# Optimization experiments

Hardware: AMD Instinct MI355X
Metric: run time of the kernel (lower is better)

Reference implementation:

```python
import jax, jax.numpy as jnp
import numpy as np

N_NODES = 100000
N_EDGES = 1600000
IN_DIM = 160
HID = 128
BN_EPS = 1e-5


def setup_inputs() -> dict:
    key = jax.random.key(0)
    ks = jax.random.split(key, 16)
    d = {}
    d['x'] = jax.random.normal(ks[0], (N_NODES, IN_DIM), dtype=jnp.float32)
    d['edge_index'] = jax.random.randint(ks[1], (2, N_EDGES), 0, N_NODES, dtype=jnp.int64)
    dims = [(IN_DIM, HID), (HID, HID), (HID, HID)]
    for i, (fi, fo) in enumerate(dims):
        s = 1.0 / np.sqrt(fi)
        d[f'wl{i}'] = jax.random.normal(ks[2 + 4 * i], (fi, fo), dtype=jnp.float32) * s
        d[f'wr{i}'] = jax.random.normal(ks[3 + 4 * i], (fi, fo), dtype=jnp.float32) * s
        d[f'bl{i}'] = jnp.zeros((fo,), dtype=jnp.float32)
        d[f'g{i}'] = jnp.ones((fo,), dtype=jnp.float32)
        d[f'be{i}'] = jnp.zeros((fo,), dtype=jnp.float32)
        d[f'rm{i}'] = jax.random.normal(ks[4 + 4 * i], (fo,), dtype=jnp.float32) * 0.1
        d[f'rv{i}'] = jnp.ones((fo,), dtype=jnp.float32)
    d['lin_w'] = jax.random.normal(ks[14], (HID, 1), dtype=jnp.float32) * (1.0 / np.sqrt(HID))
    d['lin_b'] = jnp.zeros((1,), dtype=jnp.float32)
    return d


def _sage_bn_relu(h, src, dst, wl, wr, bl, g, be, rm, rv):
    # mean neighbor aggregation: gather messages at src, scatter-mean to dst
    msg = h[src]                                            # [E, d]
    agg = jax.ops.segment_sum(msg, dst, num_segments=N_NODES)
    cnt = jax.ops.segment_sum(jnp.ones((msg.shape[0],), h.dtype), dst, num_segments=N_NODES)
    mean = agg / jnp.maximum(cnt, 1.0)[:, None]             # nodes w/o in-edges -> 0
    out = mean @ wl + bl + h @ wr                           # SAGEConv (root_weight=True)
    # BatchNorm1d (inference: running stats) + ReLU
    out = (out - rm) * (g * jax.lax.rsqrt(rv + BN_EPS)) + be
    return jax.nn.relu(out)


def reference(x, edge_index,
              wl0, wr0, bl0, g0, be0, rm0, rv0,
              wl1, wr1, bl1, g1, be1, rm1, rv1,
              wl2, wr2, bl2, g2, be2, rm2, rv2,
              lin_w, lin_b):
    src, dst = edge_index[0], edge_index[1]
    h = _sage_bn_relu(x, src, dst, wl0, wr0, bl0, g0, be0, rm0, rv0)
    h = _sage_bn_relu(h, src, dst, wl1, wr1, bl1, g1, be1, rm1, rv1)
    h = _sage_bn_relu(h, src, dst, wl2, wr2, bl2, g2, be2, rm2, rv2)
    return (h @ lin_w + lin_b)[:, 0]                        # [N]
```

## Files before the change

kernel.cpp:

```cpp
#include <hip/hip_runtime.h>

#define N_NODES 100000
#define N_EDGES 1600000
#define IN_DIM 160
#define HID 128
#define BN_EPS 1e-5f

#define M_PAD 100096
#define NBUCK 196
#define BSH 9
#define EPB 8192
#define NHB (NBUCK * NBUCK)
#define LPAD 132

typedef unsigned int uint;
typedef unsigned short ushort;
typedef __attribute__((ext_vector_type(8))) short bf16x8;
typedef __attribute__((ext_vector_type(4))) float f32x4;
typedef __attribute__((ext_vector_type(2))) float f32x2;

__device__ __forceinline__ ushort bf16rn(float f) {
    uint u = __float_as_uint(f);
    u += 0x7fffu + ((u >> 16) & 1u);
    return (ushort)(u >> 16);
}
__device__ __forceinline__ float bflo(uint u) { return __uint_as_float(u << 16); }
__device__ __forceinline__ float bfhi(uint u) { return __uint_as_float(u & 0xffff0000u); }


__device__ __forceinline__ void prep_body(int ob, int lane, const float* __restrict__ wl,
                                          const float* __restrict__ wr,
                                          ushort* __restrict__ Bf, int K) {
    int kb = ob >> 4;
    int tt = ob & 15;
    int n = tt * 16 + (lane & 15);
    int k0 = kb * 32 + (lane >> 4) * 8;
    ushort* dst = Bf + ((size_t)(kb * 16 + tt) * 64 + lane) * 8;
#pragma unroll
    for (int e = 0; e < 8; ++e) {
        int k = k0 + e;
        float v = (n < HID) ? wl[k * HID + n] : wr[k * HID + (n - HID)];
        dst[e] = bf16rn(v);
    }
}

#define PREP0_B 20
#define PREP1_B 16
#define INIT_GRID (NBUCK + PREP0_B + 2 * PREP1_B + 2)

__global__ __launch_bounds__(256) void init_kernel(
    const int* __restrict__ dst, int* __restrict__ ghist,
    const float* __restrict__ wl0, const float* __restrict__ wr0,
    const float* __restrict__ wl1, const float* __restrict__ wr1,
    const float* __restrict__ wl2, const float* __restrict__ wr2,
    ushort* __restrict__ Bf0, ushort* __restrict__ Bf1, ushort* __restrict__ Bf2,
    const float* __restrict__ bl0, const float* __restrict__ g0,
    const float* __restrict__ be0, const float* __restrict__ rm0,
    const float* __restrict__ rv0,
    const float* __restrict__ bl1, const float* __restrict__ g1,
    const float* __restrict__ be1, const float* __restrict__ rm1,
    const float* __restrict__ rv1,
    const float* __restrict__ bl2, const float* __restrict__ g2,
    const float* __restrict__ be2, const float* __restrict__ rm2,
    const float* __restrict__ rv2,
    float* __restrict__ bnscale, float* __restrict__ bnshift) {
    __shared__ int hist[NBUCK];
    int b = blockIdx.x, t = threadIdx.x;
    if (b < NBUCK) {
        for (int i = t; i < NBUCK; i += 256) hist[i] = 0;
        __syncthreads();
        int e0 = b * EPB;
        for (int i = 0; i < EPB; i += 256) {
            int e = e0 + i + t;
            if (e < N_EDGES) atomicAdd(&hist[dst[e] >> BSH], 1);
        }
        __syncthreads();
        for (int i = t; i < NBUCK; i += 256) ghist[i * NBUCK + b] = hist[i];
    } else if (b < NBUCK + PREP0_B) {
        prep_body((b - NBUCK) * 4 + (t >> 6), t & 63, wl0, wr0, Bf0, IN_DIM);
    } else if (b < NBUCK + PREP0_B + PREP1_B) {
        prep_body((b - NBUCK - PREP0_B) * 4 + (t >> 6), t & 63, wl1, wr1, Bf1, HID);
    } else if (b < NBUCK + PREP0_B + 2 * PREP1_B) {
        prep_body((b - NBUCK - PREP0_B - PREP1_B) * 4 + (t >> 6), t & 63, wl2, wr2, Bf2, HID);
    } else {
        int tt = (b - (NBUCK + PREP0_B + 2 * PREP1_B)) * 256 + t;
        if (tt < 3 * HID) {
            int L = tt >> 7, j = tt & 127;
            const float* bl = (L == 0) ? bl0 : (L == 1) ? bl1 : bl2;
            const float* gg = (L == 0) ? g0  : (L == 1) ? g1  : g2;
            const float* be = (L == 0) ? be0 : (L == 1) ? be1 : be2;
            const float* rm = (L == 0) ? rm0 : (L == 1) ? rm1 : rm2;
            const float* rv = (L == 0) ? rv0 : (L == 1) ? rv1 : rv2;
            float s = gg[j] * rsqrtf(rv[j] + BN_EPS);
            bnscale[tt] = s;
            bnshift[tt] = (bl[j] - rm[j]) * s + be[j];
        }
    }
}

#define SPT 38

__global__ __launch_bounds__(1024) void scan_all_kernel(int* __restrict__ ghist,
                                                        int* __restrict__ gbb) {
    __shared__ int ts[1024];
    int t = threadIdx.x;
    int base = t * SPT;
    int v[SPT];
    int s = 0;
#pragma unroll
    for (int i = 0; i < SPT; ++i) {
        int idx = base + i;
        int x = (idx < NHB) ? ghist[idx] : 0;
        v[i] = s;
        s += x;
    }
    ts[t] = s;
    __syncthreads();
    for (int off = 1; off < 1024; off <<= 1) {
        int a = (t >= off) ? ts[t - off] : 0;
        __syncthreads();
        ts[t] += a;
        __syncthreads();
    }
    int ex = (t > 0) ? ts[t - 1] : 0;
#pragma unroll
    for (int i = 0; i < SPT; ++i) {
        int idx = base + i;
        if (idx < NHB) {
            int e = ex + v[i];
            ghist[idx] = e;
            if (idx % NBUCK == 0) gbb[idx / NBUCK] = e;
        }
    }
    if (t == 0) gbb[NBUCK] = N_EDGES;
}


__global__ __launch_bounds__(256) void bucket_csr_kernel(const uint* __restrict__ scat,
                                                         const int* __restrict__ gbb,
                                                         int* __restrict__ prow,
                                                         int* __restrict__ deg,
                                                         int* __restrict__ peidx) {
    __shared__ int cnt[512], fl[512], pref[512];
    __shared__ int ts[256];
    __shared__ int tot_s;
    int b = blockIdx.x, t = threadIdx.x;
    int beg = gbb[b], end = gbb[b + 1];
    int pb = beg + b * 8192;
    cnt[t] = 0; cnt[t + 256] = 0;
    __syncthreads();
    for (int i = beg + t; i < end; i += 256)
        atomicAdd(&cnt[scat[i] >> 17], 1);
    __syncthreads();
    int c0 = cnt[2 * t], c1 = cnt[2 * t + 1];
    int p0 = (c0 + 15) & ~15, p1 = (c1 + 15) & ~15;
    ts[t] = p0 + p1;
    __syncthreads();
    for (int off = 1; off < 256; off <<= 1) {
        int v = (t >= off) ? ts[t - off] : 0;
        __syncthreads();
        ts[t] += v;
        __syncthreads();
    }
    int ex = (t > 0) ? ts[t - 1] : 0;
    pref[2 * t] = ex;
    pref[2 * t + 1] = ex + p0;
    fl[t] = 0; fl[t + 256] = 0;
    if (t == 255) tot_s = ts[255];
    int g0 = b * 512 + 2 * t;
    if (g0 < N_NODES) { prow[g0] = pb + ex; deg[g0] = c0; }
    if (g0 + 1 < N_NODES) { prow[g0 + 1] = pb + ex + p0; deg[g0 + 1] = c1; }
    __syncthreads();
    int tot = tot_s;
    for (int i = t; i < tot; i += 256) peidx[pb + i] = N_NODES;
    __syncthreads();
    for (int i = beg + t; i < end; i += 256) {
        uint w = scat[i];
        int nl = (int)(w >> 17);
        int lp = atomicAdd(&fl[nl], 1);
        peidx[pb + pref[nl] + lp] = (int)(w & 0x1FFFFu);
    }
}

template <int K, bool AFP32>
__device__ __forceinline__ void gemm_body(int bx, int t, ushort* ldsA,
                                          const void* __restrict__ A_,
                                          const ushort* __restrict__ Bf,
                                          ushort* __restrict__ tl,
                                          ushort* __restrict__ troot) {
    constexpr int CPR = K / 8;
    constexpr int FULLG = CPR & ~7;
    const int m0b = bx * 64;

#pragma unroll
    for (int i = 0; i < (64 * CPR) / 256; ++i) {
        int cidx = i * 256 + t;
        int row = cidx / CPR;
        int j = cidx - row * CPR;
        bf16x8 v;
        if (AFP32) {
            const float* A = (const float*)A_;
            int m = m0b + row;
            float4 f0 = make_float4(0.f, 0.f, 0.f, 0.f), f1 = f0;
            if (m < N_NODES) {
                f0 = *(const float4*)(A + (size_t)m * K + j * 8);
                f1 = *(const float4*)(A + (size_t)m * K + j * 8 + 4);
            }
            v[0] = (short)bf16rn(f0.x); v[1] = (short)bf16rn(f0.y);
            v[2] = (short)bf16rn(f0.z); v[3] = (short)bf16rn(f0.w);
            v[4] = (short)bf16rn(f1.x); v[5] = (short)bf16rn(f1.y);
            v[6] = (short)bf16rn(f1.z); v[7] = (short)bf16rn(f1.w);
        } else {
            const ushort* A = (const ushort*)A_;
            v = *(const bf16x8*)(A + (size_t)(m0b + row) * K + j * 8);
        }
        int swz = (j < FULLG) ? ((j & ~7) | ((j ^ row) & 7))
                              : ((j & ~3) | ((j ^ row) & 3));
        *(bf16x8*)&ldsA[row * K + swz * 8] = v;
    }
    __syncthreads();

    const int lane = t & 63;
    const int wv = t >> 6;
    const int col = lane & 15;
    const int q = lane >> 4;
    const int rh = wv & 1;
    const int ch = wv >> 1;
    const int row0 = rh * 32 + col;
    f32x4 acc0[8], acc1[8];
#pragma unroll
    for (int tt = 0; tt < 8; ++tt) {
        acc0[tt] = (f32x4){0.f, 0.f, 0.f, 0.f};
        acc1[tt] = (f32x4){0.f, 0.f, 0.f, 0.f};
    }

#pragma unroll
    for (int kb = 0; kb < K / 32; ++kb) {
        int jj = kb * 4 + q;
        int swzj = (jj < FULLG) ? ((jj & ~7) | ((jj ^ col) & 7))
                                : ((jj & ~3) | ((jj ^ col) & 3));
        bf16x8 a0 = *(const bf16x8*)&ldsA[row0 * K + swzj * 8];
        bf16x8 a1 = *(const bf16x8*)&ldsA[(row0 + 16) * K + swzj * 8];
        const ushort* bp = Bf + ((size_t)((kb * 16 + ch * 8) * 64) + lane) * 8;
#pragma unroll
        for (int tt = 0; tt < 8; ++tt) {
            bf16x8 bfr = *(const bf16x8*)(bp + (size_t)tt * 64 * 8);
            acc0[tt] = __builtin_amdgcn_mfma_f32_16x16x32_bf16(a0, bfr, acc0[tt], 0, 0, 0);
            acc1[tt] = __builtin_amdgcn_mfma_f32_16x16x32_bf16(a1, bfr, acc1[tt], 0, 0, 0);
        }
    }

    __syncthreads();
    ushort(*rp)[16][LPAD] = (ushort(*)[16][LPAD])ldsA;
    ushort* outp = ch ? troot : tl;
#pragma unroll
    for (int mt = 0; mt < 2; ++mt) {
        const f32x4* ac = mt ? acc1 : acc0;
#pragma unroll
        for (int tt = 0; tt < 8; ++tt)
#pragma unroll
            for (int r = 0; r < 4; ++r)
                rp[wv][q * 4 + r][tt * 16 + col] = bf16rn(ac[tt][r]);
        int mbase = m0b + rh * 32 + mt * 16;
#pragma unroll
        for (int i = 0; i < 4; ++i) {
            int lin = i * 64 + lane;
            int row = lin >> 4;
            int c16 = lin & 15;
            bf16x8 v = *(const bf16x8*)&rp[wv][row][c16 * 8];
            *(bf16x8*)(outp + (size_t)(mbase + row) * HID + c16 * 8) = v;
        }
    }
}

__global__ __launch_bounds__(256) void scatter_gemm1_kernel(
    const int* __restrict__ src, const int* __restrict__ dst,
    const int* __restrict__ ghist, uint* __restrict__ scat,
    const float* __restrict__ x, const ushort* __restrict__ Bf0,
    ushort* __restrict__ tl, ushort* __restrict__ troot) {
    constexpr int LDSE = (64 * IN_DIM > 4 * 16 * LPAD) ? 64 * IN_DIM : 4 * 16 * LPAD;
    __shared__ ushort ldsA[LDSE];
    int b = blockIdx.x, t = threadIdx.x;
    if (b < NBUCK) {
        int* base = (int*)ldsA;
        int* fill = base + NBUCK;
        for (int i = t; i < NBUCK; i += 256) { base[i] = ghist[i * NBUCK + b]; fill[i] = 0; }
        __syncthreads();
        int e0 = b * EPB;
        for (int i = 0; i < EPB; i += 256) {
            int e = e0 + i + t;
            if (e < N_EDGES) {
                int d = dst[e];
                int sv = src[e];
                int bk = d >> BSH;
                int lp = atomicAdd(&fill[bk], 1);
                scat[base[bk] + lp] = (uint)sv | ((uint)(d & 511) << 17);
            }
        }
    } else {
        gemm_body<IN_DIM, true>(b - NBUCK, t, ldsA, x, Bf0, tl, troot);
    }
}

__global__ __launch_bounds__(256) void fused_agg_gemm_kernel(
    const ushort* __restrict__ tl_in, const ushort* __restrict__ troot_in,
    const int* __restrict__ prow, const int* __restrict__ deg_,
    const int* __restrict__ peidx,
    const float* __restrict__ bnscale, const float* __restrict__ bnshift,
    const ushort* __restrict__ Bf,
    ushort* __restrict__ tl_out, ushort* __restrict__ troot_out) {
    constexpr int K = HID;
    constexpr int LDSE = (64 * K > 4 * 16 * LPAD) ? 64 * K : 4 * 16 * LPAD;
    __shared__ ushort ldsA[LDSE];
    const int t = threadIdx.x;
    const int lane = t & 63;
    const int wv = t >> 6;
    const int m0b = blockIdx.x * 64;
    const int g = lane >> 4;
    const int s = lane & 15;
    const int gsel = (lane & 48) << 2;

    for (int r = 0; r < 4; ++r) {
        const int row = wv * 16 + r * 4 + g;
        const int n = m0b + row;
        const bool valid = (n < N_NODES);
        const int nn = valid ? n : 0;
        int pbeg = prow[nn];
        int dg = valid ? deg_[nn] : 0;
        int myb = (dg + 15) >> 4;

        f32x2 acc2[4];
#pragma unroll
        for (int i = 0; i < 4; ++i) acc2[i] = (f32x2){0.f, 0.f};

        bool act = (0 < myb);
        int idx = act ? peidx[pbeg + s] : N_NODES;
        int b = 0;
        while (__any(act)) {
            uint4 u[8];
#pragma unroll
            for (int jj = 0; jj < 8; ++jj) {
                int srcj = __builtin_amdgcn_ds_bpermute(gsel | (jj << 2), idx);
                u[jj] = *(const uint4*)(tl_in + (size_t)srcj * HID + s * 8);
            }
#pragma unroll
            for (int jj = 0; jj < 8; ++jj) {
                acc2[0] += (f32x2){bflo(u[jj].x), bfhi(u[jj].x)};
                acc2[1] += (f32x2){bflo(u[jj].y), bfhi(u[jj].y)};
                acc2[2] += (f32x2){bflo(u[jj].z), bfhi(u[jj].z)};
                acc2[3] += (f32x2){bflo(u[jj].w), bfhi(u[jj].w)};
            }
#pragma unroll
            for (int jj = 0; jj < 8; ++jj) {
                int srcj = __builtin_amdgcn_ds_bpermute(gsel | ((jj + 8) << 2), idx);
                u[jj] = *(const uint4*)(tl_in + (size_t)srcj * HID + s * 8);
            }
            ++b;
            bool actn = (b < myb);
            int idxn = actn ? peidx[pbeg + b * 16 + s] : N_NODES;
#pragma unroll
            for (int jj = 0; jj < 8; ++jj) {
                acc2[0] += (f32x2){bflo(u[jj].x), bfhi(u[jj].x)};
                acc2[1] += (f32x2){bflo(u[jj].y), bfhi(u[jj].y)};
                acc2[2] += (f32x2){bflo(u[jj].z), bfhi(u[jj].z)};
                acc2[3] += (f32x2){bflo(u[jj].w), bfhi(u[jj].w)};
            }
            act = actn; idx = idxn;
        }

        float inv = 1.0f / (float)((dg > 0) ? dg : 1);
        uint4 rv = *(const uint4*)(troot_in + (size_t)nn * HID + s * 8);
        float4 sc0 = *(const float4*)(bnscale + s * 8);
        float4 sc1 = *(const float4*)(bnscale + s * 8 + 4);
        float4 sh0 = *(const float4*)(bnshift + s * 8);
        float4 sh1 = *(const float4*)(bnshift + s * 8 + 4);
        float vm = valid ? 1.0f : 0.0f;
        float o[8];
        o[0] = fmaxf(fmaf(fmaf(acc2[0].x, inv, bflo(rv.x)), sc0.x, sh0.x), 0.f) * vm;
        o[1] = fmaxf(fmaf(fmaf(acc2[0].y, inv, bfhi(rv.x)), sc0.y, sh0.y), 0.f) * vm;
        o[2] = fmaxf(fmaf(fmaf(acc2[1].x, inv, bflo(rv.y)), sc0.z, sh0.z), 0.f) * vm;
        o[3] = fmaxf(fmaf(fmaf(acc2[1].y, inv, bfhi(rv.y)), sc0.w, sh0.w), 0.f) * vm;
        o[4] = fmaxf(fmaf(fmaf(acc2[2].x, inv, bflo(rv.z)), sc1.x, sh1.x), 0.f) * vm;
        o[5] = fmaxf(fmaf(fmaf(acc2[2].y, inv, bfhi(rv.z)), sc1.y, sh1.y), 0.f) * vm;
        o[6] = fmaxf(fmaf(fmaf(acc2[3].x, inv, bflo(rv.w)), sc1.z, sh1.z), 0.f) * vm;
        o[7] = fmaxf(fmaf(fmaf(acc2[3].y, inv, bfhi(rv.w)), sc1.w, sh1.w), 0.f) * vm;

        bf16x8 pk;
#pragma unroll
        for (int e = 0; e < 8; ++e) pk[e] = (short)bf16rn(o[e]);
        int swz = (s & ~7) | ((s ^ row) & 7);
        *(bf16x8*)&ldsA[row * K + swz * 8] = pk;
    }
    __syncthreads();

    const int col = lane & 15;
    const int q = lane >> 4;
    const int rh = wv & 1;
    const int ch = wv >> 1;
    const int row0 = rh * 32 + col;
    f32x4 acc0[8], acc1[8];
#pragma unroll
    for (int tt = 0; tt < 8; ++tt) {
        acc0[tt] = (f32x4){0.f, 0.f, 0.f, 0.f};
        acc1[tt] = (f32x4){0.f, 0.f, 0.f, 0.f};
    }
#pragma unroll
    for (int kb = 0; kb < K / 32; ++kb) {
        int jj = kb * 4 + q;
        int swzj = (jj & ~7) | ((jj ^ col) & 7);
        bf16x8 a0 = *(const bf16x8*)&ldsA[row0 * K + swzj * 8];
        bf16x8 a1 = *(const bf16x8*)&ldsA[(row0 + 16) * K + swzj * 8];
        const ushort* bp = Bf + ((size_t)((kb * 16 + ch * 8) * 64) + lane) * 8;
#pragma unroll
        for (int tt = 0; tt < 8; ++tt) {
            bf16x8 bfr = *(const bf16x8*)(bp + (size_t)tt * 64 * 8);
            acc0[tt] = __builtin_amdgcn_mfma_f32_16x16x32_bf16(a0, bfr, acc0[tt], 0, 0, 0);
            acc1[tt] = __builtin_amdgcn_mfma_f32_16x16x32_bf16(a1, bfr, acc1[tt], 0, 0, 0);
        }
    }

    __syncthreads();
    ushort(*rp)[16][LPAD] = (ushort(*)[16][LPAD])ldsA;
    ushort* outp = ch ? troot_out : tl_out;
#pragma unroll
    for (int mt = 0; mt < 2; ++mt) {
        const f32x4* ac = mt ? acc1 : acc0;
#pragma unroll
        for (int tt = 0; tt < 8; ++tt)
#pragma unroll
            for (int rr = 0; rr < 4; ++rr)
                rp[wv][q * 4 + rr][tt * 16 + col] = bf16rn(ac[tt][rr]);
        int mbase = m0b + rh * 32 + mt * 16;
#pragma unroll
        for (int i = 0; i < 4; ++i) {
            int lin = i * 64 + lane;
            int rowi = lin >> 4;
            int c16 = lin & 15;
            bf16x8 v = *(const bf16x8*)&rp[wv][rowi][c16 * 8];
            *(bf16x8*)(outp + (size_t)(mbase + rowi) * HID + c16 * 8) = v;
        }
    }
}

__global__ __launch_bounds__(256) void agg_final_kernel(
    const ushort* __restrict__ tl_, const ushort* __restrict__ troot_,
    const int* __restrict__ prow, const int* __restrict__ deg_,
    const int* __restrict__ peidx,
    const float* __restrict__ bnscale, const float* __restrict__ bnshift,
    const float* __restrict__ linw, const float* __restrict__ linb,
    float* __restrict__ out) {
    const int lane = threadIdx.x & 63;
    const int wvg = (blockIdx.x * 256 + (int)threadIdx.x) >> 6;
    const int g = lane >> 4;
    const int s = lane & 15;
    const int n = wvg * 4 + g;

    int pbeg = prow[n];
    int dg = deg_[n];
    int myb = (dg + 15) >> 4;

    f32x2 acc2[4];
#pragma unroll
    for (int i = 0; i < 4; ++i) acc2[i] = (f32x2){0.f, 0.f};

    const int gsel = (lane & 48) << 2;

    bool act = (0 < myb);
    int idx = act ? peidx[pbeg + s] : N_NODES;
    int b = 0;
    while (__any(act)) {
        uint4 u[16];
#pragma unroll
        for (int jj = 0; jj < 16; ++jj) {
            int srcj = __builtin_amdgcn_ds_bpermute(gsel | (jj << 2), idx);
            u[jj] = *(const uint4*)(tl_ + (size_t)srcj * HID + s * 8);
        }
        ++b;
        bool actn = (b < myb);
        int idxn = actn ? peidx[pbeg + b * 16 + s] : N_NODES;
#pragma unroll
        for (int jj = 0; jj < 16; ++jj) {
            acc2[0] += (f32x2){bflo(u[jj].x), bfhi(u[jj].x)};
            acc2[1] += (f32x2){bflo(u[jj].y), bfhi(u[jj].y)};
            acc2[2] += (f32x2){bflo(u[jj].z), bfhi(u[jj].z)};
            acc2[3] += (f32x2){bflo(u[jj].w), bfhi(u[jj].w)};
        }
        act = actn; idx = idxn;
    }

    float inv = 1.0f / (float)((dg > 0) ? dg : 1);
    uint4 rv = *(const uint4*)(troot_ + (size_t)n * HID + s * 8);
    float4 sc0 = *(const float4*)(bnscale + s * 8);
    float4 sc1 = *(const float4*)(bnscale + s * 8 + 4);
    float4 sh0 = *(const float4*)(bnshift + s * 8);
    float4 sh1 = *(const float4*)(bnshift + s * 8 + 4);
    float o[8];
    o[0] = fmaxf(fmaf(fmaf(acc2[0].x, inv, bflo(rv.x)), sc0.x, sh0.x), 0.f);
    o[1] = fmaxf(fmaf(fmaf(acc2[0].y, inv, bfhi(rv.x)), sc0.y, sh0.y), 0.f);
    o[2] = fmaxf(fmaf(fmaf(acc2[1].x, inv, bflo(rv.y)), sc0.z, sh0.z), 0.f);
    o[3] = fmaxf(fmaf(fmaf(acc2[1].y, inv, bfhi(rv.y)), sc0.w, sh0.w), 0.f);
    o[4] = fmaxf(fmaf(fmaf(acc2[2].x, inv, bflo(rv.z)), sc1.x, sh1.x), 0.f);
    o[5] = fmaxf(fmaf(fmaf(acc2[2].y, inv, bfhi(rv.z)), sc1.y, sh1.y), 0.f);
    o[6] = fmaxf(fmaf(fmaf(acc2[3].x, inv, bflo(rv.w)), sc1.z, sh1.z), 0.f);
    o[7] = fmaxf(fmaf(fmaf(acc2[3].y, inv, bfhi(rv.w)), sc1.w, sh1.w), 0.f);

    float4 w0 = *(const float4*)(linw + s * 8);
    float4 w1 = *(const float4*)(linw + s * 8 + 4);
    float p = o[0] * w0.x + o[1] * w0.y + o[2] * w0.z + o[3] * w0.w +
              o[4] * w1.x + o[5] * w1.y + o[6] * w1.z + o[7] * w1.w;
#pragma unroll
    for (int off = 1; off < 16; off <<= 1) p += __shfl_xor(p, off);
    if (s == 0) out[n] = p + linb[0];
}


extern "C" void kernel_launch(void* const* d_in, const int* in_sizes, int n_in,
                              void* d_out, int out_size, void* d_ws, size_t ws_size,
                              hipStream_t stream) {
    const float* x    = (const float*)d_in[0];
    const int*   ei   = (const int*)d_in[1];
    const int*   esrc = ei;
    const int*   edst = ei + N_EDGES;
    const float* wl[3]; const float* wr[3]; const float* bl[3];
    const float* g[3];  const float* be[3]; const float* rm[3]; const float* rv[3];
    for (int i = 0; i < 3; ++i) {
        wl[i] = (const float*)d_in[2 + 7 * i];
        wr[i] = (const float*)d_in[3 + 7 * i];
        bl[i] = (const float*)d_in[4 + 7 * i];
        g[i]  = (const float*)d_in[5 + 7 * i];
        be[i] = (const float*)d_in[6 + 7 * i];
        rm[i] = (const float*)d_in[7 + 7 * i];
        rv[i] = (const float*)d_in[8 + 7 * i];
    }
    const float* lin_w = (const float*)d_in[23];
    const float* lin_b = (const float*)d_in[24];
    float* out = (float*)d_out;

    char* ws = (char*)d_ws;
    size_t off = 0;
    auto carve = [&](size_t bytes) -> void* {
        void* p = ws + off;
        off += (bytes + 255) & ~(size_t)255;
        return p;
    };
    int*    prow   = (int*)carve((size_t)(N_NODES + 8) * sizeof(int));
    int*    deg    = (int*)carve((size_t)(N_NODES + 8) * sizeof(int));
    int*    peidx  = (int*)carve((size_t)3210000 * sizeof(int));
    uint*   scat   = (uint*)carve((size_t)N_EDGES * sizeof(uint));
    int*    ghist  = (int*)carve((size_t)(NHB + 256) * sizeof(int));
    int*    gbb    = (int*)carve((NBUCK + 4) * sizeof(int));
    ushort* tl0    = (ushort*)carve((size_t)(M_PAD + 1) * HID * sizeof(ushort));
    ushort* troot0 = (ushort*)carve((size_t)M_PAD * HID * sizeof(ushort));
    ushort* tl1    = (ushort*)carve((size_t)(M_PAD + 1) * HID * sizeof(ushort));
    ushort* troot1 = (ushort*)carve((size_t)M_PAD * HID * sizeof(ushort));
    ushort* Bf0    = (ushort*)carve(256 * IN_DIM * sizeof(ushort));
    ushort* Bf1    = (ushort*)carve(256 * HID * sizeof(ushort));
    ushort* Bf2    = (ushort*)carve(256 * HID * sizeof(ushort));
    float*  bnsc   = (float*)carve(3 * HID * sizeof(float));
    float*  bnsh   = (float*)carve(3 * HID * sizeof(float));
    (void)ws_size; (void)n_in; (void)in_sizes; (void)out_size;

    const int GEMM_GRID = M_PAD / 64;
    const int AGGF_GRID = N_NODES / 16;

    init_kernel<<<INIT_GRID, 256, 0, stream>>>(
        edst, ghist,
        wl[0], wr[0], wl[1], wr[1], wl[2], wr[2], Bf0, Bf1, Bf2,
        bl[0], g[0], be[0], rm[0], rv[0],
        bl[1], g[1], be[1], rm[1], rv[1],
        bl[2], g[2], be[2], rm[2], rv[2],
        bnsc, bnsh);
    scan_all_kernel<<<1, 1024, 0, stream>>>(ghist, gbb);
    scatter_gemm1_kernel<<<NBUCK + GEMM_GRID, 256, 0, stream>>>(
        esrc, edst, ghist, scat, x, Bf0, tl0, troot0);
    bucket_csr_kernel<<<NBUCK, 256, 0, stream>>>(scat, gbb, prow, deg, peidx);

    fused_agg_gemm_kernel<<<GEMM_GRID, 256, 0, stream>>>(
        tl0, troot0, prow, deg, peidx, bnsc, bnsh, Bf1, tl1, troot1);
    fused_agg_gemm_kernel<<<GEMM_GRID, 256, 0, stream>>>(
        tl1, troot1, prow, deg, peidx, bnsc + HID, bnsh + HID, Bf2, tl0, troot0);
    agg_final_kernel<<<AGGF_GRID, 256, 0, stream>>>(
        tl0, troot0, prow, deg, peidx, bnsc + 2 * HID, bnsh + 2 * HID,
        lin_w, lin_b, out);
}
```

Baseline: 463.0 us.

## Fold scan into init, slice final layer features, widen gather batch

Merges the histogram scan into the init kernel's last block via an atomic done counter, which removes one kernel launch. The second fused layer now writes its outputs in a feature-sliced layout of 16 columns per slice. The final aggregation kernel runs eight blocks per node chunk, each gathering one slice, and combines the partial dot products with atomicAdd into an output zeroed by memset. The gather loop in fused_agg_gemm issues 16 neighbor loads before accumulating, and BN constants are hoisted out of the row loop. The sliced layout is meant to improve cache locality of the last gather, at the cost of atomics, two extra memsets, and nondeterministic float summation order.

```diff
diff --git a/kernel.cpp b/kernel.cpp
--- a/kernel.cpp
+++ b/kernel.cpp
@@ -18,6 +18,7 @@
 typedef __attribute__((ext_vector_type(8))) short bf16x8;
 typedef __attribute__((ext_vector_type(4))) float f32x4;
 typedef __attribute__((ext_vector_type(2))) float f32x2;
+typedef __attribute__((ext_vector_type(4))) uint uint4v;
 
 __device__ __forceinline__ ushort bf16rn(float f) {
     uint u = __float_as_uint(f);
@@ -49,7 +50,8 @@
 #define INIT_GRID (NBUCK + PREP0_B + 2 * PREP1_B + 2)
 
 __global__ __launch_bounds__(256) void init_kernel(
-    const int* __restrict__ dst, int* __restrict__ ghist,
+    const int* __restrict__ dst, int* __restrict__ ghist, int* __restrict__ gbb,
+    int* __restrict__ done_ctr,
     const float* __restrict__ wl0, const float* __restrict__ wr0,
     const float* __restrict__ wl1, const float* __restrict__ wr1,
     const float* __restrict__ wl2, const float* __restrict__ wr2,
@@ -65,6 +67,8 @@
     const float* __restrict__ rv2,
     float* __restrict__ bnscale, float* __restrict__ bnshift) {
     __shared__ int hist[NBUCK];
+    __shared__ int ts2[256];
+    __shared__ int is_last;
     int b = blockIdx.x, t = threadIdx.x;
     if (b < NBUCK) {
         for (int i = t; i < NBUCK; i += 256) hist[i] = 0;
@@ -96,40 +100,44 @@
             bnshift[tt] = (bl[j] - rm[j]) * s + be[j];
         }
     }
-}
-
-#define SPT 38
-
-__global__ __launch_bounds__(1024) void scan_all_kernel(int* __restrict__ ghist,
-                                                        int* __restrict__ gbb) {
-    __shared__ int ts[1024];
-    int t = threadIdx.x;
-    int base = t * SPT;
-    int v[SPT];
+    __threadfence();
+    if (t == 0) is_last = (atomicAdd(done_ctr, 1) == INIT_GRID - 1);
+    __syncthreads();
+    if (!is_last) return;
+    __threadfence();
+    int base4 = t * 38;
     int s = 0;
 #pragma unroll
-    for (int i = 0; i < SPT; ++i) {
-        int idx = base + i;
-        int x = (idx < NHB) ? ghist[idx] : 0;
-        v[i] = s;
-        s += x;
-    }
-    ts[t] = s;
-    __syncthreads();
-    for (int off = 1; off < 1024; off <<= 1) {
-        int a = (t >= off) ? ts[t - off] : 0;
+    for (int i = 0; i < 38; ++i) {
+        int i4 = base4 + i;
+        if (i4 * 4 < NHB) {
+            int4 v = ((const int4*)ghist)[i4];
+            s += v.x + v.y + v.z + v.w;
+        }
+    }
+    ts2[t] = s;
+    __syncthreads();
+    for (int off = 1; off < 256; off <<= 1) {
+        int a = (t >= off) ? ts2[t - off] : 0;
         __syncthreads();
-        ts[t] += a;
+        ts2[t] += a;
         __syncthreads();
     }
-    int ex = (t > 0) ? ts[t - 1] : 0;
-#pragma unroll
-    for (int i = 0; i < SPT; ++i) {
-        int idx = base + i;
-        if (idx < NHB) {
-            int e = ex + v[i];
-            ghist[idx] = e;
-            if (idx % NBUCK == 0) gbb[idx / NBUCK] = e;
+    int run = (t > 0) ? ts2[t - 1] : 0;
+#pragma unroll
+    for (int i = 0; i < 38; ++i) {
+        int i4 = base4 + i;
+        if (i4 * 4 < NHB) {
+            int4 v = ((const int4*)ghist)[i4];
+            int4 w;
+            w.x = run;
+            w.y = w.x + v.x;
+            w.z = w.y + v.y;
+            w.w = w.z + v.z;
+            run = w.w + v.w;
+            ((int4*)ghist)[i4] = w;
+            int idx = i4 * 4;
+            if (idx % NBUCK == 0) gbb[idx / NBUCK] = w.x;
         }
     }
     if (t == 0) gbb[NBUCK] = N_EDGES;
@@ -302,6 +310,7 @@
     }
 }
 
+template <bool SLICED_OUT>
 __global__ __launch_bounds__(256) void fused_agg_gemm_kernel(
     const ushort* __restrict__ tl_in, const ushort* __restrict__ troot_in,
     const int* __restrict__ prow, const int* __restrict__ deg_,
@@ -320,6 +329,11 @@
     const int s = lane & 15;
     const int gsel = (lane & 48) << 2;
 
+    float4 sc0 = *(const float4*)(bnscale + s * 8);
+    float4 sc1 = *(const float4*)(bnscale + s * 8 + 4);
+    float4 sh0 = *(const float4*)(bnshift + s * 8);
+    float4 sh1 = *(const float4*)(bnshift + s * 8 + 4);
+
     for (int r = 0; r < 4; ++r) {
         const int row = wv * 16 + r * 4 + g;
         const int n = m0b + row;
@@ -337,29 +351,17 @@
         int idx = act ? peidx[pbeg + s] : N_NODES;
         int b = 0;
         while (__any(act)) {
-            uint4 u[8];
-#pragma unroll
-            for (int jj = 0; jj < 8; ++jj) {
+            uint4 u[16];
+#pragma unroll
+            for (int jj = 0; jj < 16; ++jj) {
                 int srcj = __builtin_amdgcn_ds_bpermute(gsel | (jj << 2), idx);
-                u[jj] = *(const uint4*)(tl_in + (size_t)srcj * HID + s * 8);
-            }
-#pragma unroll
-            for (int jj = 0; jj < 8; ++jj) {
-                acc2[0] += (f32x2){bflo(u[jj].x), bfhi(u[jj].x)};
-                acc2[1] += (f32x2){bflo(u[jj].y), bfhi(u[jj].y)};
-                acc2[2] += (f32x2){bflo(u[jj].z), bfhi(u[jj].z)};
-                acc2[3] += (f32x2){bflo(u[jj].w), bfhi(u[jj].w)};
-            }
-#pragma unroll
-            for (int jj = 0; jj < 8; ++jj) {
-                int srcj = __builtin_amdgcn_ds_bpermute(gsel | ((jj + 8) << 2), idx);
                 u[jj] = *(const uint4*)(tl_in + (size_t)srcj * HID + s * 8);
             }
             ++b;
             bool actn = (b < myb);
             int idxn = actn ? peidx[pbeg + b * 16 + s] : N_NODES;
 #pragma unroll
-            for (int jj = 0; jj < 8; ++jj) {
+            for (int jj = 0; jj < 16; ++jj) {
                 acc2[0] += (f32x2){bflo(u[jj].x), bfhi(u[jj].x)};
                 acc2[1] += (f32x2){bflo(u[jj].y), bfhi(u[jj].y)};
                 acc2[2] += (f32x2){bflo(u[jj].z), bfhi(u[jj].z)};
@@ -370,10 +372,6 @@
 
         float inv = 1.0f / (float)((dg > 0) ? dg : 1);
         uint4 rv = *(const uint4*)(troot_in + (size_t)nn * HID + s * 8);
-        float4 sc0 = *(const float4*)(bnscale + s * 8);
-        float4 sc1 = *(const float4*)(bnscale + s * 8 + 4);
-        float4 sh0 = *(const float4*)(bnshift + s * 8);
-        float4 sh1 = *(const float4*)(bnshift + s * 8 + 4);
         float vm = valid ? 1.0f : 0.0f;
         float o[8];
         o[0] = fmaxf(fmaf(fmaf(acc2[0].x, inv, bflo(rv.x)), sc0.x, sh0.x), 0.f) * vm;
@@ -431,86 +429,102 @@
             for (int rr = 0; rr < 4; ++rr)
                 rp[wv][q * 4 + rr][tt * 16 + col] = bf16rn(ac[tt][rr]);
         int mbase = m0b + rh * 32 + mt * 16;
-#pragma unroll
-        for (int i = 0; i < 4; ++i) {
-            int lin = i * 64 + lane;
-            int rowi = lin >> 4;
-            int c16 = lin & 15;
-            bf16x8 v = *(const bf16x8*)&rp[wv][rowi][c16 * 8];
-            *(bf16x8*)(outp + (size_t)(mbase + rowi) * HID + c16 * 8) = v;
+        if (SLICED_OUT) {
+#pragma unroll
+            for (int i = 0; i < 4; ++i) {
+                int unit = i * 64 + lane;
+                int sl = unit >> 5;
+                int rw = (unit >> 1) & 15;
+                int hf = unit & 1;
+                bf16x8 v = *(const bf16x8*)&rp[wv][rw][sl * 16 + hf * 8];
+                *(bf16x8*)(outp + ((size_t)sl * M_PAD + (mbase + rw)) * 16 + hf * 8) = v;
+            }
+        } else {
+#pragma unroll
+            for (int i = 0; i < 4; ++i) {
+                int lin = i * 64 + lane;
+                int rowi = lin >> 4;
+                int c16 = lin & 15;
+                bf16x8 v = *(const bf16x8*)&rp[wv][rowi][c16 * 8];
+                *(bf16x8*)(outp + (size_t)(mbase + rowi) * HID + c16 * 8) = v;
+            }
         }
     }
 }
 
 __global__ __launch_bounds__(256) void agg_final_kernel(
-    const ushort* __restrict__ tl_, const ushort* __restrict__ troot_,
+    const ushort* __restrict__ tls, const ushort* __restrict__ troots,
     const int* __restrict__ prow, const int* __restrict__ deg_,
     const int* __restrict__ peidx,
     const float* __restrict__ bnscale, const float* __restrict__ bnshift,
     const float* __restrict__ linw, const float* __restrict__ linb,
     float* __restrict__ out) {
-    const int lane = threadIdx.x & 63;
-    const int wvg = (blockIdx.x * 256 + (int)threadIdx.x) >> 6;
+    const int t = threadIdx.x;
+    const int lane = t & 63;
+    const int wv = t >> 6;
+    const int sl = blockIdx.x & 7;
+    const int chunk = blockIdx.x >> 3;
     const int g = lane >> 4;
-    const int s = lane & 15;
-    const int n = wvg * 4 + g;
-
-    int pbeg = prow[n];
-    int dg = deg_[n];
-    int myb = (dg + 15) >> 4;
+    const int j = lane & 15;
+    const int k = j >> 1;
+    const int hf = j & 1;
+    const int n = chunk * 16 + wv * 4 + g;
+    const size_t sb = (size_t)sl * M_PAD;
+
+    int pbeg = __builtin_nontemporal_load(prow + n);
+    int dg = __builtin_nontemporal_load(deg_ + n);
+    int myb = ((dg + 15) >> 4) * 2;
 
     f32x2 acc2[4];
 #pragma unroll
     for (int i = 0; i < 4; ++i) acc2[i] = (f32x2){0.f, 0.f};
 
-    const int gsel = (lane & 48) << 2;
-
+    const ushort* tb = tls + sb * 16;
     bool act = (0 < myb);
-    int idx = act ? peidx[pbeg + s] : N_NODES;
     int b = 0;
     while (__any(act)) {
-        uint4 u[16];
-#pragma unroll
-        for (int jj = 0; jj < 16; ++jj) {
-            int srcj = __builtin_amdgcn_ds_bpermute(gsel | (jj << 2), idx);
-            u[jj] = *(const uint4*)(tl_ + (size_t)srcj * HID + s * 8);
-        }
+        int src = act ? __builtin_nontemporal_load(peidx + pbeg + b * 8 + k) : N_NODES;
+        uint4 u = *(const uint4*)(tb + (size_t)src * 16 + hf * 8);
+        acc2[0] += (f32x2){bflo(u.x), bfhi(u.x)};
+        acc2[1] += (f32x2){bflo(u.y), bfhi(u.y)};
+        acc2[2] += (f32x2){bflo(u.z), bfhi(u.z)};
+        acc2[3] += (f32x2){bflo(u.w), bfhi(u.w)};
         ++b;
-        bool actn = (b < myb);
-        int idxn = actn ? peidx[pbeg + b * 16 + s] : N_NODES;
-#pragma unroll
-        for (int jj = 0; jj < 16; ++jj) {
-            acc2[0] += (f32x2){bflo(u[jj].x), bfhi(u[jj].x)};
-            acc2[1] += (f32x2){bflo(u[jj].y), bfhi(u[jj].y)};
-            acc2[2] += (f32x2){bflo(u[jj].z), bfhi(u[jj].z)};
-            acc2[3] += (f32x2){bflo(u[jj].w), bfhi(u[jj].w)};
-        }
-        act = actn; idx = idxn;
+        act = (b < myb);
+    }
+
+#pragma unroll
+    for (int i = 0; i < 4; ++i) {
+#pragma unroll
+        for (int off = 2; off <= 8; off <<= 1) {
+            acc2[i].x += __shfl_xor(acc2[i].x, off);
+            acc2[i].y += __shfl_xor(acc2[i].y, off);
+        }
     }
 
     float inv = 1.0f / (float)((dg > 0) ? dg : 1);
-    uint4 rv = *(const uint4*)(troot_ + (size_t)n * HID + s * 8);
-    float4 sc0 = *(const float4*)(bnscale + s * 8);
-    float4 sc1 = *(const float4*)(bnscale + s * 8 + 4);
-    float4 sh0 = *(const float4*)(bnshift + s * 8);
-    float4 sh1 = *(const float4*)(bnshift + s * 8 + 4);
+    int fb = sl * 16 + hf * 8;
+    uint4v rv = __builtin_nontemporal_load((const uint4v*)(troots + (sb + n) * 16 + hf * 8));
+    float4 sc0 = *(const float4*)(bnscale + fb);
+    float4 sc1 = *(const float4*)(bnscale + fb + 4);
+    float4 sh0 = *(const float4*)(bnshift + fb);
+    float4 sh1 = *(const float4*)(bnshift + fb + 4);
     float o[8];
-    o[0] = fmaxf(fmaf(fmaf(acc2[0].x, inv, bflo(rv.x)), sc0.x, sh0.x), 0.f);
-    o[1] = fmaxf(fmaf(fmaf(acc2[0].y, inv, bfhi(rv.x)), sc0.y, sh0.y), 0.f);
-    o[2] = fmaxf(fmaf(fmaf(acc2[1].x, inv, bflo(rv.y)), sc0.z, sh0.z), 0.f);
-    o[3] = fmaxf(fmaf(fmaf(acc2[1].y, inv, bfhi(rv.y)), sc0.w, sh0.w), 0.f);
-    o[4] = fmaxf(fmaf(fmaf(acc2[2].x, inv, bflo(rv.z)), sc1.x, sh1.x), 0.f);
-    o[5] = fmaxf(fmaf(fmaf(acc2[2].y, inv, bfhi(rv.z)), sc1.y, sh1.y), 0.f);
-    o[6] = fmaxf(fmaf(fmaf(acc2[3].x, inv, bflo(rv.w)), sc1.z, sh1.z), 0.f);
-    o[7] = fmaxf(fmaf(fmaf(acc2[3].y, inv, bfhi(rv.w)), sc1.w, sh1.w), 0.f);
-
-    float4 w0 = *(const float4*)(linw + s * 8);
-    float4 w1 = *(const float4*)(linw + s * 8 + 4);
+    o[0] = fmaxf(fmaf(fmaf(acc2[0].x, inv, bflo(rv[0])), sc0.x, sh0.x), 0.f);
+    o[1] = fmaxf(fmaf(fmaf(acc2[0].y, inv, bfhi(rv[0])), sc0.y, sh0.y), 0.f);
+    o[2] = fmaxf(fmaf(fmaf(acc2[1].x, inv, bflo(rv[1])), sc0.z, sh0.z), 0.f);
+    o[3] = fmaxf(fmaf(fmaf(acc2[1].y, inv, bfhi(rv[1])), sc0.w, sh0.w), 0.f);
+    o[4] = fmaxf(fmaf(fmaf(acc2[2].x, inv, bflo(rv[2])), sc1.x, sh1.x), 0.f);
+    o[5] = fmaxf(fmaf(fmaf(acc2[2].y, inv, bfhi(rv[2])), sc1.y, sh1.y), 0.f);
+    o[6] = fmaxf(fmaf(fmaf(acc2[3].x, inv, bflo(rv[3])), sc1.z, sh1.z), 0.f);
+    o[7] = fmaxf(fmaf(fmaf(acc2[3].y, inv, bfhi(rv[3])), sc1.w, sh1.w), 0.f);
+
+    float4 w0 = *(const float4*)(linw + fb);
+    float4 w1 = *(const float4*)(linw + fb + 4);
     float p = o[0] * w0.x + o[1] * w0.y + o[2] * w0.z + o[3] * w0.w +
               o[4] * w1.x + o[5] * w1.y + o[6] * w1.z + o[7] * w1.w;
-#pragma unroll
-    for (int off = 1; off < 16; off <<= 1) p += __shfl_xor(p, off);
-    if (s == 0) out[n] = p + linb[0];
+    p += __shfl_xor(p, 1);
+    if (j == 0) atomicAdd(out + n, p + ((sl == 0) ? linb[0] : 0.f));
 }
 
 
@@ -549,10 +563,11 @@
     uint*   scat   = (uint*)carve((size_t)N_EDGES * sizeof(uint));
     int*    ghist  = (int*)carve((size_t)(NHB + 256) * sizeof(int));
     int*    gbb    = (int*)carve((NBUCK + 4) * sizeof(int));
+    int*    done   = (int*)carve(16 * sizeof(int));
     ushort* tl0    = (ushort*)carve((size_t)(M_PAD + 1) * HID * sizeof(ushort));
-    ushort* troot0 = (ushort*)carve((size_t)M_PAD * HID * sizeof(ushort));
+    ushort* troot0 = (ushort*)carve((size_t)(M_PAD + 1) * HID * sizeof(ushort));
     ushort* tl1    = (ushort*)carve((size_t)(M_PAD + 1) * HID * sizeof(ushort));
-    ushort* troot1 = (ushort*)carve((size_t)M_PAD * HID * sizeof(ushort));
+    ushort* troot1 = (ushort*)carve((size_t)(M_PAD + 1) * HID * sizeof(ushort));
     ushort* Bf0    = (ushort*)carve(256 * IN_DIM * sizeof(ushort));
     ushort* Bf1    = (ushort*)carve(256 * HID * sizeof(ushort));
     ushort* Bf2    = (ushort*)carve(256 * HID * sizeof(ushort));
@@ -561,23 +576,25 @@
     (void)ws_size; (void)n_in; (void)in_sizes; (void)out_size;
 
     const int GEMM_GRID = M_PAD / 64;
-    const int AGGF_GRID = N_NODES / 16;
+    const int AGGF_GRID = 8 * (N_NODES / 16);
+
+    hipMemsetAsync(done, 0, sizeof(int), stream);
+    hipMemsetAsync(out, 0, (size_t)N_NODES * sizeof(float), stream);
 
     init_kernel<<<INIT_GRID, 256, 0, stream>>>(
-        edst, ghist,
+        edst, ghist, gbb, done,
         wl[0], wr[0], wl[1], wr[1], wl[2], wr[2], Bf0, Bf1, Bf2,
         bl[0], g[0], be[0], rm[0], rv[0],
         bl[1], g[1], be[1], rm[1], rv[1],
         bl[2], g[2], be[2], rm[2], rv[2],
         bnsc, bnsh);
-    scan_all_kernel<<<1, 1024, 0, stream>>>(ghist, gbb);
     scatter_gemm1_kernel<<<NBUCK + GEMM_GRID, 256, 0, stream>>>(
         esrc, edst, ghist, scat, x, Bf0, tl0, troot0);
     bucket_csr_kernel<<<NBUCK, 256, 0, stream>>>(scat, gbb, prow, deg, peidx);
 
-    fused_agg_gemm_kernel<<<GEMM_GRID, 256, 0, stream>>>(
+    fused_agg_gemm_kernel<false><<<GEMM_GRID, 256, 0, stream>>>(
         tl0, troot0, prow, deg, peidx, bnsc, bnsh, Bf1, tl1, troot1);
-    fused_agg_gemm_kernel<<<GEMM_GRID, 256, 0, stream>>>(
+    fused_agg_gemm_kernel<true><<<GEMM_GRID, 256, 0, stream>>>(
         tl1, troot1, prow, deg, peidx, bnsc + HID, bnsh + HID, Bf2, tl0, troot0);
     agg_final_kernel<<<AGGF_GRID, 256, 0, stream>>>(
         tl0, troot0, prow, deg, peidx, bnsc + 2 * HID, bnsh + 2 * HID,
```

New measurement: 573.5 us. +23.9%, slower.
